# Kernel tuning notes

Measured on AMD Instinct MI355X. Metric: run time of the kernel, lower is better.

Reference implementation:

```python
import jax, jax.numpy as jnp
import numpy as np

B, R, S = 4, 16384, 96
NEAR, FAR = 2.0, 6.0

def setup_inputs() -> dict:
    key = jax.random.key(0)
    k1, k2, k3 = jax.random.split(key, 3)
    colors = jax.random.normal(k1, (B, R, S, 3), dtype=jnp.float32)
    densities = jax.random.normal(k2, (B, R, S, 1), dtype=jnp.float32)
    # depths must be monotonically increasing along the sample axis
    depths = jnp.sort(
        NEAR + (FAR - NEAR) * jax.random.uniform(k3, (B, R, S, 1), dtype=jnp.float32),
        axis=2,
    )
    return {"colors": colors, "densities": densities, "depths": depths, "white_back": 0}


def reference(colors, densities, depths, white_back):
    dtype = colors.dtype
    # midpoint (Mip-NeRF style) quantities along the sample axis (dim 2)
    deltas = depths[:, :, 1:] - depths[:, :, :-1]            # [B,R,S-1,1]
    colors_mid = (colors[:, :, :-1] + colors[:, :, 1:]) * 0.5  # [B,R,S-1,3]
    densities_mid = (densities[:, :, :-1] + densities[:, :, 1:]) * 0.5
    depths_mid = (depths[:, :, :-1] + depths[:, :, 1:]) * 0.5

    densities_mid = jax.nn.softplus(densities_mid).astype(dtype)  # activation_factory
    density_delta = densities_mid * deltas
    alpha = (1.0 - jnp.exp(-density_delta)).astype(dtype)         # [B,R,S-1,1]

    # transmittance via cumulative product of shifted (1 - alpha)
    alpha_shifted = jnp.concatenate(
        [jnp.ones_like(alpha[:, :, :1]), 1.0 - alpha + 1e-10], axis=2
    )
    weights = (alpha * jnp.cumprod(alpha_shifted, axis=2)[:, :, :-1]).astype(dtype)

    composite_rgb = jnp.sum(weights * colors_mid, axis=2)   # [B,R,3]
    weight_total = jnp.sum(weights, axis=2)                 # [B,R,1]
    composite_depth = jnp.sum(weights * depths_mid, axis=2) # [B,R,1]
    composite_depth = jnp.nan_to_num(composite_depth, nan=jnp.inf).astype(dtype)
    composite_depth = jnp.clip(composite_depth, jnp.min(depths), jnp.max(depths))

    if white_back:
        composite_rgb = composite_rgb + 1.0 - weight_total
    return composite_rgb, composite_depth, weights
```

## Files before the change

### kernel.cpp

```cpp
#include <hip/hip_runtime.h>
#include <math.h>

#define S 96
#define SM 95
#define RPW 8
#define L2E 1.4426950408889634f

__device__ __forceinline__ float fexp2(float x) {
#if __has_builtin(__builtin_amdgcn_exp2f)
    return __builtin_amdgcn_exp2f(x);
#else
    return exp2f(x);
#endif
}
__device__ __forceinline__ float flog2(float x) {
#if __has_builtin(__builtin_amdgcn_logf)
    return __builtin_amdgcn_logf(x);
#else
    return log2f(x);
#endif
}

template <int CTRL, int RMASK>
__device__ __forceinline__ float updpp0(float src) {
    return __int_as_float(__builtin_amdgcn_update_dpp(
        0, __float_as_int(src), CTRL, RMASK, 0xF, false));
}

__device__ __forceinline__ float dpp_scan_add(float x) {
    x += updpp0<0x111, 0xF>(x);
    x += updpp0<0x112, 0xF>(x);
    x += updpp0<0x114, 0xF>(x);
    x += updpp0<0x118, 0xF>(x);
    x += updpp0<0x142, 0xA>(x);
    x += updpp0<0x143, 0xC>(x);
    return x;
}

__device__ __forceinline__ float rdlane(float x, int lane) {
    return __int_as_float(__builtin_amdgcn_readlane(__float_as_int(x), lane));
}
__device__ __forceinline__ float wave_sum(float x) {
    return rdlane(dpp_scan_add(x), 63);
}
__device__ __forceinline__ float wshr1(float x) { return updpp0<0x138, 0xF>(x); }
__device__ __forceinline__ float wshl1(float x) { return updpp0<0x130, 0xF>(x); }

__global__ void init_ws_kernel(unsigned int* ws) {
    ws[0] = 0x7F800000u;
    ws[1] = 0xFF800000u;
}

template <bool SLOT>
__global__ __launch_bounds__(256) void march_kernel(
    const float* __restrict__ colors,
    const float* __restrict__ dens,
    const float* __restrict__ depths,
    const int* __restrict__ white_back,
    unsigned int* __restrict__ ws,
    float* __restrict__ out_rgb,
    float* __restrict__ out_dep,
    float* __restrict__ out_w,
    int nrays, int nblocks) {
    const int wv = threadIdx.x >> 6;
    const int l = threadIdx.x & 63;
    const int waveId = blockIdx.x * 4 + wv;
    const int wb = *white_back;
    const float C1 = 0.5f * L2E;

    float mn = INFINITY, mx = -INFINITY;

#pragma unroll 2
    for (int it = 0; it < RPW; ++it) {
        const int ray = waveId * RPW + it;
        if (ray >= nrays) break;

        const float* db = depths + (size_t)ray * S;
        const float* sb = dens + (size_t)ray * S;
        const float* cb = colors + (size_t)ray * (3 * S);

        float d_a = db[l];
        float s_a = sb[l];
        float c0_a = cb[3 * l + 0];
        float c1_a = cb[3 * l + 1];
        float c2_a = cb[3 * l + 2];
        const bool hb = (l < 32);
        float d_b = hb ? db[64 + l] : 0.f;
        float s_b = hb ? sb[64 + l] : 0.f;
        float c0_b = hb ? cb[192 + 3 * l + 0] : 0.f;
        float c1_b = hb ? cb[192 + 3 * l + 1] : 0.f;
        float c2_b = hb ? cb[192 + 3 * l + 2] : 0.f;

        mn = fminf(mn, rdlane(d_a, 0));
        mx = fmaxf(mx, rdlane(d_b, 31));

        float dn_a = wshl1(d_a);
        float sn_a = wshl1(s_a);
        {
            float d64 = rdlane(d_b, 0);
            float s64 = rdlane(s_b, 0);
            if (l == 63) { dn_a = d64; sn_a = s64; }
        }
        float dn_b = wshl1(d_b);
        float sn_b = wshl1(s_b);

        float x_a = (s_a + sn_a) * C1;
        float lg_a = fmaxf(x_a, 0.f) + flog2(1.f + fexp2(-fabsf(x_a)));
        float dd_a = (dn_a - d_a) * lg_a;
        float x_b = (s_b + sn_b) * C1;
        float lg_b = fmaxf(x_b, 0.f) + flog2(1.f + fexp2(-fabsf(x_b)));
        float dd_b = (l <= 30) ? (dn_b - d_b) * lg_b : 0.f;

        float A = dpp_scan_add(dd_a);
        float P = rdlane(A, 63);
        float Bc = dpp_scan_add(dd_b);

        float Ti_a = fexp2(-A);
        float Ti_b = fexp2(-(P + Bc));
        float T63 = rdlane(Ti_a, 62);
        float T64 = rdlane(Ti_a, 63);
        float T95 = rdlane(Ti_b, 31);

        float Te_a = wshr1(Ti_a);
        if (l == 0) Te_a = 1.f;
        float Te_b = wshr1(Ti_b);
        if (l == 0) Te_b = T64;
        float Tm1_a = wshr1(Te_a);
        if (l == 0) Tm1_a = 1.f;
        float Tm1_b = wshr1(Te_b);
        if (l == 0) Tm1_b = T63;

        float w_a = Te_a - Ti_a;
        float w_b = Te_b - Ti_b;
        float v_a = 0.5f * (Tm1_a - Ti_a);
        float v_b = hb ? 0.5f * (Tm1_b - Ti_b) : 0.f;

        float r_sum = wave_sum(v_a * c0_a + v_b * c0_b);
        float g_sum = wave_sum(v_a * c1_a + v_b * c1_b);
        float b_sum = wave_sum(v_a * c2_a + v_b * c2_b);
        float dep_sum = wave_sum(v_a * d_a + v_b * d_b);

        float* wout = out_w + (size_t)ray * SM;
        wout[l] = w_a;
        if (l <= 30) wout[64 + l] = w_b;

        if (l == 0) {
            float rr = r_sum, gg = g_sum, bb = b_sum;
            if (wb) { rr += T95; gg += T95; bb += T95; }
            out_rgb[(size_t)ray * 3 + 0] = rr;
            out_rgb[(size_t)ray * 3 + 1] = gg;
            out_rgb[(size_t)ray * 3 + 2] = bb;
            float cd = dep_sum;
            if (isnan(cd)) cd = INFINITY;
            out_dep[ray] = cd;
        }
    }

    __shared__ float smn[4], smx[4];
    if (l == 0) { smn[wv] = mn; smx[wv] = mx; }
    __syncthreads();
    if (threadIdx.x == 0) {
        float bmn = fminf(fminf(smn[0], smn[1]), fminf(smn[2], smn[3]));
        float bmx = fmaxf(fmaxf(smx[0], smx[1]), fmaxf(smx[2], smx[3]));
        if (SLOT) {
            float* sl = (float*)ws;
            sl[2 + blockIdx.x] = bmn;
            sl[2 + nblocks + blockIdx.x] = bmx;
        } else {
            atomicMin((int*)&ws[0], __float_as_int(bmn));
            atomicMax((int*)&ws[1], __float_as_int(bmx));
        }
    }
}

__global__ __launch_bounds__(256) void tail_kernel(
    float* __restrict__ dep, const unsigned int* __restrict__ ws,
    int n, int nblocks, int slotMode) {
    float gmn, gmx;
    if (slotMode) {
        const float* sl = (const float*)ws + 2;
        float mn = INFINITY, mx = -INFINITY;
        for (int i = threadIdx.x; i < nblocks; i += 256) {
            mn = fminf(mn, sl[i]);
            mx = fmaxf(mx, sl[i + nblocks]);
        }
#pragma unroll
        for (int off = 32; off >= 1; off >>= 1) {
            mn = fminf(mn, __shfl_xor(mn, off));
            mx = fmaxf(mx, __shfl_xor(mx, off));
        }
        __shared__ float a[4], b[4];
        const int wv = threadIdx.x >> 6;
        if ((threadIdx.x & 63) == 0) { a[wv] = mn; b[wv] = mx; }
        __syncthreads();
        gmn = fminf(fminf(a[0], a[1]), fminf(a[2], a[3]));
        gmx = fmaxf(fmaxf(b[0], b[1]), fmaxf(b[2], b[3]));
    } else {
        gmn = __int_as_float((int)ws[0]);
        gmx = __int_as_float((int)ws[1]);
    }
    int i = blockIdx.x * 256 + threadIdx.x;
    if (i < n) dep[i] = fminf(fmaxf(dep[i], gmn), gmx);
}

extern "C" void kernel_launch(void* const* d_in, const int* in_sizes, int n_in,
                              void* d_out, int out_size, void* d_ws, size_t ws_size,
                              hipStream_t stream) {
    const float* colors = (const float*)d_in[0];
    const float* dens = (const float*)d_in[1];
    const float* depths = (const float*)d_in[2];
    const int* white_back = (const int*)d_in[3];

    const int nrays = in_sizes[1] / S;
    unsigned int* ws = (unsigned int*)d_ws;

    float* out_rgb = (float*)d_out;
    float* out_dep = out_rgb + (size_t)nrays * 3;
    float* out_w = out_dep + nrays;

    const int raysPerBlock = RPW * 4;
    const int nblocks = (nrays + raysPerBlock - 1) / raysPerBlock;
    const bool slot = ws_size >= (size_t)(2 + 2 * nblocks) * sizeof(float);

    if (slot) {
        march_kernel<true><<<nblocks, 256, 0, stream>>>(
            colors, dens, depths, white_back, ws, out_rgb, out_dep, out_w,
            nrays, nblocks);
    } else {
        init_ws_kernel<<<1, 1, 0, stream>>>(ws);
        march_kernel<false><<<nblocks, 256, 0, stream>>>(
            colors, dens, depths, white_back, ws, out_rgb, out_dep, out_w,
            nrays, nblocks);
    }
    tail_kernel<<<(nrays + 255) / 256, 256, 0, stream>>>(
        out_dep, ws, nrays, nblocks, slot ? 1 : 0);
}
```

Baseline: 36.07 us.

## Map one ray per thread with sequential scan and LDS-staged weight stores

Replaces the wave-per-ray layout with a thread-per-ray layout. Each thread loads its samples as double-buffered float4 tiles and does the transmittance scan serially instead of with DPP wave scans. Weights are staged in shared memory and written out cooperatively as float4 to keep stores coalesced. The cost is per-thread strided global loads, a large LDS footprint and only one wave per block, which may reduce latency hiding for a bandwidth-bound kernel.

```diff
diff --git a/kernel.cpp b/kernel.cpp
--- a/kernel.cpp
+++ b/kernel.cpp
@@ -3,7 +3,7 @@
 
 #define S 96
 #define SM 95
-#define RPW 8
+#define TS 12
 #define L2E 1.4426950408889634f
 
 __device__ __forceinline__ float fexp2(float x) {
@@ -21,30 +21,24 @@
 #endif
 }
 
-template <int CTRL, int RMASK>
-__device__ __forceinline__ float updpp0(float src) {
-    return __int_as_float(__builtin_amdgcn_update_dpp(
-        0, __float_as_int(src), CTRL, RMASK, 0xF, false));
-}
-
-__device__ __forceinline__ float dpp_scan_add(float x) {
-    x += updpp0<0x111, 0xF>(x);
-    x += updpp0<0x112, 0xF>(x);
-    x += updpp0<0x114, 0xF>(x);
-    x += updpp0<0x118, 0xF>(x);
-    x += updpp0<0x142, 0xA>(x);
-    x += updpp0<0x143, 0xC>(x);
-    return x;
-}
-
-__device__ __forceinline__ float rdlane(float x, int lane) {
-    return __int_as_float(__builtin_amdgcn_readlane(__float_as_int(x), lane));
-}
-__device__ __forceinline__ float wave_sum(float x) {
-    return rdlane(dpp_scan_add(x), 63);
-}
-__device__ __forceinline__ float wshr1(float x) { return updpp0<0x138, 0xF>(x); }
-__device__ __forceinline__ float wshl1(float x) { return updpp0<0x130, 0xF>(x); }
+__device__ __forceinline__ float f4c(const float4& v, int i) {
+    return i == 0 ? v.x : i == 1 ? v.y : i == 2 ? v.z : v.w;
+}
+
+struct Tile {
+    float4 d[3], s[3], c[9];
+};
+
+__device__ __forceinline__ void load_tile(Tile& T, const float4* dv,
+                                          const float4* sv, const float4* cv,
+                                          int tl) {
+#pragma unroll
+    for (int k = 0; k < 3; ++k) T.d[k] = dv[tl * 3 + k];
+#pragma unroll
+    for (int k = 0; k < 3; ++k) T.s[k] = sv[tl * 3 + k];
+#pragma unroll
+    for (int k = 0; k < 9; ++k) T.c[k] = cv[tl * 9 + k];
+}
 
 __global__ void init_ws_kernel(unsigned int* ws) {
     ws[0] = 0x7F800000u;
@@ -52,7 +46,7 @@
 }
 
 template <bool SLOT>
-__global__ __launch_bounds__(256) void march_kernel(
+__global__ __launch_bounds__(64) void march_kernel(
     const float* __restrict__ colors,
     const float* __restrict__ dens,
     const float* __restrict__ depths,
@@ -62,115 +56,103 @@
     float* __restrict__ out_dep,
     float* __restrict__ out_w,
     int nrays, int nblocks) {
-    const int wv = threadIdx.x >> 6;
-    const int l = threadIdx.x & 63;
-    const int waveId = blockIdx.x * 4 + wv;
-    const int wb = *white_back;
+    __shared__ float wlds[64 * SM];
+
+    const int t = threadIdx.x;
+    const int ray = blockIdx.x * 64 + t;
+    const bool act = (ray < nrays);
+    const int rayc = act ? ray : (nrays - 1);
+
+    const float4* dv = (const float4*)(depths + (size_t)rayc * S);
+    const float4* sv = (const float4*)(dens + (size_t)rayc * S);
+    const float4* cv = (const float4*)(colors + (size_t)rayc * (3 * S));
+
     const float C1 = 0.5f * L2E;
-
-    float mn = INFINITY, mx = -INFINITY;
-
-#pragma unroll 2
-    for (int it = 0; it < RPW; ++it) {
-        const int ray = waveId * RPW + it;
-        if (ray >= nrays) break;
-
-        const float* db = depths + (size_t)ray * S;
-        const float* sb = dens + (size_t)ray * S;
-        const float* cb = colors + (size_t)ray * (3 * S);
-
-        float d_a = db[l];
-        float s_a = sb[l];
-        float c0_a = cb[3 * l + 0];
-        float c1_a = cb[3 * l + 1];
-        float c2_a = cb[3 * l + 2];
-        const bool hb = (l < 32);
-        float d_b = hb ? db[64 + l] : 0.f;
-        float s_b = hb ? sb[64 + l] : 0.f;
-        float c0_b = hb ? cb[192 + 3 * l + 0] : 0.f;
-        float c1_b = hb ? cb[192 + 3 * l + 1] : 0.f;
-        float c2_b = hb ? cb[192 + 3 * l + 2] : 0.f;
-
-        mn = fminf(mn, rdlane(d_a, 0));
-        mx = fmaxf(mx, rdlane(d_b, 31));
-
-        float dn_a = wshl1(d_a);
-        float sn_a = wshl1(s_a);
-        {
-            float d64 = rdlane(d_b, 0);
-            float s64 = rdlane(s_b, 0);
-            if (l == 63) { dn_a = d64; sn_a = s64; }
-        }
-        float dn_b = wshl1(d_b);
-        float sn_b = wshl1(s_b);
-
-        float x_a = (s_a + sn_a) * C1;
-        float lg_a = fmaxf(x_a, 0.f) + flog2(1.f + fexp2(-fabsf(x_a)));
-        float dd_a = (dn_a - d_a) * lg_a;
-        float x_b = (s_b + sn_b) * C1;
-        float lg_b = fmaxf(x_b, 0.f) + flog2(1.f + fexp2(-fabsf(x_b)));
-        float dd_b = (l <= 30) ? (dn_b - d_b) * lg_b : 0.f;
-
-        float A = dpp_scan_add(dd_a);
-        float P = rdlane(A, 63);
-        float Bc = dpp_scan_add(dd_b);
-
-        float Ti_a = fexp2(-A);
-        float Ti_b = fexp2(-(P + Bc));
-        float T63 = rdlane(Ti_a, 62);
-        float T64 = rdlane(Ti_a, 63);
-        float T95 = rdlane(Ti_b, 31);
-
-        float Te_a = wshr1(Ti_a);
-        if (l == 0) Te_a = 1.f;
-        float Te_b = wshr1(Ti_b);
-        if (l == 0) Te_b = T64;
-        float Tm1_a = wshr1(Te_a);
-        if (l == 0) Tm1_a = 1.f;
-        float Tm1_b = wshr1(Te_b);
-        if (l == 0) Tm1_b = T63;
-
-        float w_a = Te_a - Ti_a;
-        float w_b = Te_b - Ti_b;
-        float v_a = 0.5f * (Tm1_a - Ti_a);
-        float v_b = hb ? 0.5f * (Tm1_b - Ti_b) : 0.f;
-
-        float r_sum = wave_sum(v_a * c0_a + v_b * c0_b);
-        float g_sum = wave_sum(v_a * c1_a + v_b * c1_b);
-        float b_sum = wave_sum(v_a * c2_a + v_b * c2_b);
-        float dep_sum = wave_sum(v_a * d_a + v_b * d_b);
-
-        float* wout = out_w + (size_t)ray * SM;
-        wout[l] = w_a;
-        if (l <= 30) wout[64 + l] = w_b;
-
-        if (l == 0) {
-            float rr = r_sum, gg = g_sum, bb = b_sum;
-            if (wb) { rr += T95; gg += T95; bb += T95; }
-            out_rgb[(size_t)ray * 3 + 0] = rr;
-            out_rgb[(size_t)ray * 3 + 1] = gg;
-            out_rgb[(size_t)ray * 3 + 2] = bb;
-            float cd = dep_sum;
-            if (isnan(cd)) cd = INFINITY;
-            out_dep[ray] = cd;
-        }
-    }
-
-    __shared__ float smn[4], smx[4];
-    if (l == 0) { smn[wv] = mn; smx[wv] = mx; }
-    __syncthreads();
-    if (threadIdx.x == 0) {
-        float bmn = fminf(fminf(smn[0], smn[1]), fminf(smn[2], smn[3]));
-        float bmx = fmaxf(fmaxf(smx[0], smx[1]), fmaxf(smx[2], smx[3]));
+    float run = 0.f, Tp = 1.f;
+    float racc = 0.f, gacc = 0.f, bacc = 0.f, dacc = 0.f;
+
+    Tile A, B;
+    load_tile(A, dv, sv, cv, 0);
+    float d_p = A.d[0].x, s_p = A.s[0].x;
+    float c0_p = A.c[0].x, c1_p = A.c[0].y, c2_p = A.c[0].z;
+    const float dmin0 = d_p;
+
+    auto compute = [&](const Tile& T, int base, bool skip0) {
+#pragma unroll
+        for (int k = 0; k < TS; ++k) {
+            if (skip0 && k == 0) continue;
+            float dc = f4c(T.d[k >> 2], k & 3);
+            float sc = f4c(T.s[k >> 2], k & 3);
+            float c0 = f4c(T.c[(3 * k) >> 2], (3 * k) & 3);
+            float c1 = f4c(T.c[(3 * k + 1) >> 2], (3 * k + 1) & 3);
+            float c2 = f4c(T.c[(3 * k + 2) >> 2], (3 * k + 2) & 3);
+            float x2 = (s_p + sc) * C1;
+            float sp = fmaxf(x2, 0.f) + flog2(1.f + fexp2(-fabsf(x2)));
+            run += (dc - d_p) * sp;
+            float Tc = fexp2(-run);
+            float w = Tp - Tc;
+            racc += w * (c0_p + c0);
+            gacc += w * (c1_p + c1);
+            bacc += w * (c2_p + c2);
+            dacc += w * (d_p + dc);
+            wlds[t * SM + (base + k - 1)] = w;
+            d_p = dc; s_p = sc; c0_p = c0; c1_p = c1; c2_p = c2; Tp = Tc;
+        }
+    };
+
+    load_tile(B, dv, sv, cv, 1);
+    compute(A, 0, true);
+    load_tile(A, dv, sv, cv, 2);
+    compute(B, 12, false);
+    load_tile(B, dv, sv, cv, 3);
+    compute(A, 24, false);
+    load_tile(A, dv, sv, cv, 4);
+    compute(B, 36, false);
+    load_tile(B, dv, sv, cv, 5);
+    compute(A, 48, false);
+    load_tile(A, dv, sv, cv, 6);
+    compute(B, 60, false);
+    load_tile(B, dv, sv, cv, 7);
+    compute(A, 72, false);
+    compute(B, 84, false);
+
+    if (act) {
+        float T95 = Tp;
+        float rr = 0.5f * racc, gg = 0.5f * gacc, bb = 0.5f * bacc;
+        if (*white_back) { rr += T95; gg += T95; bb += T95; }
+        out_rgb[(size_t)ray * 3 + 0] = rr;
+        out_rgb[(size_t)ray * 3 + 1] = gg;
+        out_rgb[(size_t)ray * 3 + 2] = bb;
+        float cd = 0.5f * dacc;
+        if (isnan(cd)) cd = INFINITY;
+        out_dep[ray] = cd;
+    }
+
+    float mn = act ? dmin0 : INFINITY;
+    float mx = act ? d_p : -INFINITY;
+#pragma unroll
+    for (int off = 32; off >= 1; off >>= 1) {
+        mn = fminf(mn, __shfl_xor(mn, off));
+        mx = fmaxf(mx, __shfl_xor(mx, off));
+    }
+    if (t == 0) {
         if (SLOT) {
             float* sl = (float*)ws;
-            sl[2 + blockIdx.x] = bmn;
-            sl[2 + nblocks + blockIdx.x] = bmx;
+            sl[2 + blockIdx.x] = mn;
+            sl[2 + nblocks + blockIdx.x] = mx;
         } else {
-            atomicMin((int*)&ws[0], __float_as_int(bmn));
-            atomicMax((int*)&ws[1], __float_as_int(bmx));
-        }
-    }
+            atomicMin((int*)&ws[0], __float_as_int(mn));
+            atomicMax((int*)&ws[1], __float_as_int(mx));
+        }
+    }
+
+    __syncthreads();
+    const int totalF = (min(64, nrays - blockIdx.x * 64)) * SM;
+    float* wdst = out_w + (size_t)blockIdx.x * 64 * SM;
+    const float4* wsrc4 = (const float4*)wlds;
+    float4* wdst4 = (float4*)wdst;
+    for (int i4 = t; i4 * 4 + 3 < totalF; i4 += 64) wdst4[i4] = wsrc4[i4];
+    for (int i = (totalF & ~3) + t; i < totalF; i += 64) wdst[i] = wlds[i];
 }
 
 __global__ __launch_bounds__(256) void tail_kernel(
@@ -218,17 +200,16 @@
     float* out_dep = out_rgb + (size_t)nrays * 3;
     float* out_w = out_dep + nrays;
 
-    const int raysPerBlock = RPW * 4;
-    const int nblocks = (nrays + raysPerBlock - 1) / raysPerBlock;
+    const int nblocks = (nrays + 63) / 64;
     const bool slot = ws_size >= (size_t)(2 + 2 * nblocks) * sizeof(float);
 
     if (slot) {
-        march_kernel<true><<<nblocks, 256, 0, stream>>>(
+        march_kernel<true><<<nblocks, 64, 0, stream>>>(
             colors, dens, depths, white_back, ws, out_rgb, out_dep, out_w,
             nrays, nblocks);
     } else {
         init_ws_kernel<<<1, 1, 0, stream>>>(ws);
-        march_kernel<false><<<nblocks, 256, 0, stream>>>(
+        march_kernel<false><<<nblocks, 64, 0, stream>>>(
             colors, dens, depths, white_back, ws, out_rgb, out_dep, out_w,
             nrays, nblocks);
     }
```

After: 48.76 us. +35.2%, slower.
